# Performance work log

Measured on AMD Instinct MI355X. Metric: run time of the kernel, lower is better.

Reference implementation:

```python
import jax, jax.numpy as jnp
import numpy as np

N = 20000   # nodes
E = 320000  # edges per meta-path
F = 256     # input feature dim
H = 8       # attention heads
D = 64      # out dim per head
M = 2       # meta-paths
C = 5       # classes
HID = 128   # semantic attention hidden


def setup_inputs():
    key = jax.random.key(0)
    ks = jax.random.split(key, 12)
    s_in = 1.0 / np.sqrt(F)
    s_sem = 1.0 / np.sqrt(H * D)
    return {
        "h": jax.random.normal(ks[0], (N, F), jnp.float32),
        "src": jax.random.randint(ks[1], (M, E), 0, N, dtype=jnp.int32),
        "dst": jax.random.randint(ks[2], (M, E), 0, N, dtype=jnp.int32),
        "W": jax.random.normal(ks[3], (M, F, H * D), jnp.float32) * s_in,
        "attn_l": jax.random.normal(ks[4], (M, H, D), jnp.float32) * 0.1,
        "attn_r": jax.random.normal(ks[5], (M, H, D), jnp.float32) * 0.1,
        "bias_g": jnp.zeros((M, H * D), jnp.float32),
        "sem_W1": jax.random.normal(ks[6], (H * D, HID), jnp.float32) * s_sem,
        "sem_b1": jnp.zeros((HID,), jnp.float32),
        "sem_W2": jax.random.normal(ks[7], (HID, 1), jnp.float32) * (1.0 / np.sqrt(HID)),
        "pred_W": jax.random.normal(ks[8], (H * D, C), jnp.float32) * s_sem,
        "pred_b": jnp.zeros((C,), jnp.float32),
    }


def _gat_metapath(h, src, dst, W, al, ar, b):
    # DGL GATConv (allow_zero_in_degree=True), dropout disabled.
    feat = (h @ W).reshape(N, H, D)                     # [N,H,D]
    el = jnp.einsum("nhd,hd->nh", feat, al)             # [N,H]
    er = jnp.einsum("nhd,hd->nh", feat, ar)
    e = jax.nn.leaky_relu(el[src] + er[dst], 0.2)       # [E,H]
    # edge softmax over destination neighborhoods
    m = jax.ops.segment_max(e, dst, num_segments=N)
    m = jax.lax.stop_gradient(jnp.where(jnp.isfinite(m), m, 0.0))
    ex = jnp.exp(e - m[dst])
    den = jax.ops.segment_sum(ex, dst, num_segments=N)
    alpha = ex / jnp.maximum(den[dst], 1e-9)            # [E,H]
    # scatter-aggregate messages
    out = jax.ops.segment_sum(alpha[:, :, None] * feat[src], dst, num_segments=N)  # [N,H,D]
    out = jax.nn.elu(out + b.reshape(1, H, D))          # bias then activation (elu)
    return out.reshape(N, H * D)


def reference(h, src, dst, W, attn_l, attn_r, bias_g, sem_W1, sem_b1, sem_W2, pred_W, pred_b):
    # one GATConv per meta-path, flattened heads
    z = jnp.stack(
        [_gat_metapath(h, src[i], dst[i], W[i], attn_l[i], attn_r[i], bias_g[i]) for i in range(M)],
        axis=1,
    )  # [N, M, H*D]
    # semantic attention pooling over meta-paths
    w = jnp.tanh(z @ sem_W1 + sem_b1) @ sem_W2          # [N,M,1]
    beta = jax.nn.softmax(w.mean(0), axis=0)            # [M,1]
    hout = (beta[None] * z).sum(1)                      # [N,H*D]
    return hout @ pred_W + pred_b                        # [N,C]
```

## Files before the change

### kernel.cpp

```cpp
#include <hip/hip_runtime.h>
#include <hip/hip_bf16.h>

#define NN  20000
#define FF  256
#define HH  8
#define DD  64
#define HD  512
#define MM  2
#define EE  320000
#define CC  5
#define HID 128

#define GEMM_BLOCKS 1252
#define LP 40

typedef __attribute__((ext_vector_type(8))) short short8;
typedef __attribute__((ext_vector_type(4))) float f32x4;

__device__ __forceinline__ short f2bs(float v) {
  __hip_bfloat16 b = __float2bfloat16(v);
  return *reinterpret_cast<short*>(&b);
}
__device__ __forceinline__ int clampi(int v, int lo, int hi) {
  return v < lo ? lo : (v > hi ? hi : v);
}
__device__ __forceinline__ void bf8_unpack(uint4 u, float f[8]) {
  f[0] = __uint_as_float(u.x << 16); f[1] = __uint_as_float(u.x & 0xffff0000u);
  f[2] = __uint_as_float(u.y << 16); f[3] = __uint_as_float(u.y & 0xffff0000u);
  f[4] = __uint_as_float(u.z << 16); f[5] = __uint_as_float(u.z & 0xffff0000u);
  f[6] = __uint_as_float(u.w << 16); f[7] = __uint_as_float(u.w & 0xffff0000u);
}

__global__ __launch_bounds__(256) void convert_k(
    const float* __restrict__ W, const float* __restrict__ W1,
    const float* __restrict__ predW, const int* __restrict__ dst,
    __hip_bfloat16* __restrict__ Wt, __hip_bfloat16* __restrict__ W1t,
    __hip_bfloat16* __restrict__ predWt, int* __restrict__ counts,
    float* __restrict__ wsum)
{
  const int bid = blockIdx.x, tid = threadIdx.x;
  __shared__ short T[64 * 65];
  if (bid < 64) {
    int m = bid >> 5, t = bid & 31;
    int k0 = (t >> 3) * 64, c0 = (t & 7) * 64;
    const float* src = W + (size_t)m * FF * HD;
#pragma unroll
    for (int rr = 0; rr < 16; ++rr) {
      int idx = rr * 256 + tid;
      int r = idx >> 6, c = idx & 63;
      T[c * 65 + r] = f2bs(src[(size_t)(k0 + r) * HD + c0 + c]);
    }
    __syncthreads();
    __hip_bfloat16* dstp = Wt + (size_t)m * HD * FF;
#pragma unroll
    for (int rr = 0; rr < 16; ++rr) {
      int idx = rr * 256 + tid;
      int c = idx >> 6, k = idx & 63;
      dstp[(size_t)(c0 + c) * FF + k0 + k] = *reinterpret_cast<__hip_bfloat16*>(&T[c * 65 + k]);
    }
  } else if (bid < 80) {
    int t = bid - 64;
    int k0 = (t >> 1) * 64, c0 = (t & 1) * 64;
#pragma unroll
    for (int rr = 0; rr < 16; ++rr) {
      int idx = rr * 256 + tid;
      int r = idx >> 6, c = idx & 63;
      T[c * 65 + r] = f2bs(W1[(size_t)(k0 + r) * HID + c0 + c]);
    }
    __syncthreads();
#pragma unroll
    for (int rr = 0; rr < 16; ++rr) {
      int idx = rr * 256 + tid;
      int c = idx >> 6, k = idx & 63;
      W1t[(size_t)(c0 + c) * HD + k0 + k] = *reinterpret_cast<__hip_bfloat16*>(&T[c * 65 + k]);
    }
  } else if (bid == 80) {
    for (int i = tid; i < 16 * HD; i += 256) {
      int c = i >> 9, k = i & 511;
      predWt[i] = __float2bfloat16((c < CC) ? predW[(size_t)k * CC + c] : 0.f);
    }
    if (tid < 64) wsum[tid] = 0.f;
  } else {
    int e = (bid - 81) * 256 + tid;
    if (e < MM * EE) {
      int m = e / EE;
      int d = clampi(dst[e], 0, NN - 1);
      atomicAdd(&counts[m * NN + d], 1);
    }
  }
}

__global__ __launch_bounds__(256) void scan_k(const int* __restrict__ counts,
                                              int* __restrict__ offsets,
                                              int* __restrict__ cursor)
{
  const int m = blockIdx.x;
  const int tid = threadIdx.x;
  const int CH = (NN + 255) / 256;
  const int lo = tid * CH;
  const int hi = min(NN, lo + CH);
  __shared__ int sdata[256];
  int s = 0;
  for (int i = lo; i < hi; ++i) s += counts[m * NN + i];
  const int own = s;
  sdata[tid] = s;
  __syncthreads();
#pragma unroll
  for (int off = 1; off < 256; off <<= 1) {
    int v = (tid >= off) ? sdata[tid - off] : 0;
    __syncthreads();
    sdata[tid] += v;
    __syncthreads();
  }
  int run = sdata[tid] - own;
  for (int i = lo; i < hi; ++i) {
    offsets[m * (NN + 1) + i] = run;
    cursor[m * NN + i] = run;
    run += counts[m * NN + i];
  }
  if (tid == 255) offsets[m * (NN + 1) + NN] = sdata[255];
}

__global__ __launch_bounds__(256) void work_k(
    const float* __restrict__ h, const __hip_bfloat16* __restrict__ Wt,
    const float* __restrict__ al, const float* __restrict__ ar,
    const int* __restrict__ dst, const int* __restrict__ src,
    int* __restrict__ cursor, int* __restrict__ sidx,
    __hip_bfloat16* __restrict__ feat, float* __restrict__ el, float* __restrict__ er)
{
  if (blockIdx.x >= GEMM_BLOCKS) {
    int e = (blockIdx.x - GEMM_BLOCKS) * 256 + (int)threadIdx.x;
    if (e < MM * EE) {
      int m = e / EE;
      int d = clampi(dst[e], 0, NN - 1);
      int pos = atomicAdd(&cursor[m * NN + d], 1);
      sidx[(size_t)m * EE + pos] = clampi(src[e], 0, NN - 1);
    }
    return;
  }
  const int m    = blockIdx.x & 1;
  const int half = (blockIdx.x >> 1) & 1;
  const int row0 = (blockIdx.x >> 2) * 64;
  const int cb   = half * 256;
  const int tid  = threadIdx.x;
  const int wave = tid >> 6, lane = tid & 63;
  const int l15  = lane & 15, quad = lane >> 4;
  __shared__ __align__(16) short As[64 * LP];
  __shared__ __align__(16) short Bs[256 * LP];
  f32x4 acc[16];
#pragma unroll
  for (int i = 0; i < 16; ++i) acc[i] = (f32x4){0.f, 0.f, 0.f, 0.f};
  const __hip_bfloat16* Wtm = Wt + (size_t)m * HD * FF;

  for (int k0 = 0; k0 < FF; k0 += 32) {
    {
      int r = tid >> 2, kg = tid & 3;
      int row = row0 + r;
      short sv[8];
      if (row < NN) {
        const float* hp = h + (size_t)row * FF + k0 + kg * 8;
        float4 x = *(const float4*)hp, y = *(const float4*)(hp + 4);
        sv[0]=f2bs(x.x); sv[1]=f2bs(x.y); sv[2]=f2bs(x.z); sv[3]=f2bs(x.w);
        sv[4]=f2bs(y.x); sv[5]=f2bs(y.y); sv[6]=f2bs(y.z); sv[7]=f2bs(y.w);
      } else {
#pragma unroll
        for (int j = 0; j < 8; ++j) sv[j] = 0;
      }
      *(uint4*)(&As[r * LP + kg * 8]) = *(uint4*)sv;
    }
#pragma unroll
    for (int jj = 0; jj < 4; ++jj) {
      int idx = jj * 256 + tid;
      int c = idx >> 2, kg = idx & 3;
      *(uint4*)(&Bs[c * LP + kg * 8]) =
          *(const uint4*)(Wtm + (size_t)(cb + c) * FF + k0 + kg * 8);
    }
    __syncthreads();
    short8 a = *(const short8*)(&As[(16 * wave + l15) * LP + quad * 8]);
#pragma unroll
    for (int nt = 0; nt < 16; ++nt) {
      short8 b = *(const short8*)(&Bs[(nt * 16 + l15) * LP + quad * 8]);
      acc[nt] = __builtin_amdgcn_mfma_f32_16x16x32_bf16(a, b, acc[nt], 0, 0, 0);
    }
    __syncthreads();
  }
#pragma unroll
  for (int nt = 0; nt < 16; ++nt)
#pragma unroll
    for (int r = 0; r < 4; ++r) {
      int row = row0 + 16 * wave + quad * 4 + r;
      if (row < NN)
        feat[(size_t)m * NN * HD + (size_t)row * HD + cb + nt * 16 + l15] =
            __float2bfloat16(acc[nt][r]);
    }
#pragma unroll
  for (int lh = 0; lh < 4; ++lh) {
    const int hh2 = half * 4 + lh;
    float alv[4], arv[4];
#pragma unroll
    for (int t = 0; t < 4; ++t) {
      size_t ai = (size_t)m * HD + hh2 * 64 + t * 16 + l15;
      alv[t] = al[ai];
      arv[t] = ar[ai];
    }
#pragma unroll
    for (int r = 0; r < 4; ++r) {
      int row = row0 + 16 * wave + quad * 4 + r;
      float sl = 0.f, sr = 0.f;
#pragma unroll
      for (int t = 0; t < 4; ++t) {
        sl += acc[lh * 4 + t][r] * alv[t];
        sr += acc[lh * 4 + t][r] * arv[t];
      }
#pragma unroll
      for (int s = 1; s < 16; s <<= 1) {
        sl += __shfl_xor(sl, s);
        sr += __shfl_xor(sr, s);
      }
      if (l15 == 0 && row < NN) {
        el[((size_t)m * NN + row) * 8 + hh2] = sl;
        er[((size_t)m * NN + row) * 8 + hh2] = sr;
      }
    }
  }
}

__global__ __launch_bounds__(512) void aggregate_k(
    const int* __restrict__ sidx, const int* __restrict__ offsets,
    const float* __restrict__ el, const float* __restrict__ er,
    const __hip_bfloat16* __restrict__ feat, const float* __restrict__ bias_g,
    __hip_bfloat16* __restrict__ z)
{
  const int m = blockIdx.y;
  const int wave = threadIdx.x >> 6, lane = threadIdx.x & 63;
  const int n = blockIdx.x * 8 + wave;
  if (n >= NN) return;
  const int hh = lane >> 3;
  const int off = offsets[m * (NN + 1) + n];
  const int end = offsets[m * (NN + 1) + n + 1];
  const float er_h = er[((size_t)m * NN + n) * 8 + hh];
  const float* elm = el + (size_t)m * NN * 8;
  const int* sx = sidx + (size_t)m * EE;
  const __hip_bfloat16* fb = feat + (size_t)m * NN * HD + lane * 8;

  float acc[8];
#pragma unroll
  for (int j = 0; j < 8; ++j) acc[j] = 0.f;
  float den = 0.f;

  for (int base = off; base < end; base += 64) {
    const int cnt = min(64, end - base);
    int s_l = 0;
    if (lane < cnt) s_l = clampi(sx[base + lane], 0, NN - 1);
    int s_cur = __shfl(s_l, 0);
    uint4 u_cur = *(const uint4*)(fb + (size_t)s_cur * HD);
    float e_cur = elm[s_cur * 8 + hh];
    for (int i = 0; i < cnt; ++i) {
      int s_nxt = 0; uint4 u_nxt; float e_nxt = 0.f;
      if (i + 1 < cnt) {
        s_nxt = __shfl(s_l, i + 1);
        u_nxt = *(const uint4*)(fb + (size_t)s_nxt * HD);
        e_nxt = elm[s_nxt * 8 + hh];
      }
      float v = e_cur + er_h;
      v = v > 0.f ? v : 0.2f * v;
      float w = __expf(v);
      den += w;
      float f[8];
      bf8_unpack(u_cur, f);
#pragma unroll
      for (int j = 0; j < 8; ++j) acc[j] += w * f[j];
      s_cur = s_nxt; u_cur = u_nxt; e_cur = e_nxt;
    }
  }
  const float invden = 1.0f / fmaxf(den, 1e-9f);
  short sv[8];
#pragma unroll
  for (int j = 0; j < 8; ++j) {
    float o = acc[j] * invden + bias_g[(size_t)m * HD + lane * 8 + j];
    o = o > 0.f ? o : expm1f(o);
    sv[j] = f2bs(o);
  }
  *(uint4*)(z + ((size_t)m * NN + n) * HD + lane * 8) = *(uint4*)sv;
}

__global__ __launch_bounds__(256) void gemm_sem_k(
    const __hip_bfloat16* __restrict__ z, const __hip_bfloat16* __restrict__ W1t,
    const __hip_bfloat16* __restrict__ predWt,
    const float* __restrict__ b1, const float* __restrict__ W2,
    float* __restrict__ wsum, float* __restrict__ y)
{
  const int row0 = blockIdx.x * 64;
  const int tid  = threadIdx.x;
  const int wave = tid >> 6, lane = tid & 63;
  const int l15  = lane & 15, quad = lane >> 4;
  __shared__ __align__(16) short As[64 * LP];
  __shared__ __align__(16) short Bs[128 * LP];
  __shared__ float s_part[2];
  if (tid < 2) s_part[tid] = 0.f;
  f32x4 acc[8], accy;
#pragma unroll
  for (int i = 0; i < 8; ++i) acc[i] = (f32x4){0.f, 0.f, 0.f, 0.f};
  accy = (f32x4){0.f, 0.f, 0.f, 0.f};

  for (int k0 = 0; k0 < HD; k0 += 32) {
    {
      int r = tid >> 2, kg = tid & 3;
      *(uint4*)(&As[r * LP + kg * 8]) =
          *(const uint4*)(z + (size_t)(row0 + r) * HD + k0 + kg * 8);
    }
#pragma unroll
    for (int jj = 0; jj < 2; ++jj) {
      int idx = jj * 256 + tid;
      int c = idx >> 2, kg = idx & 3;
      *(uint4*)(&Bs[c * LP + kg * 8]) =
          *(const uint4*)(W1t + (size_t)c * HD + k0 + kg * 8);
    }
    __syncthreads();
    short8 a = *(const short8*)(&As[(16 * wave + l15) * LP + quad * 8]);
#pragma unroll
    for (int nt = 0; nt < 8; ++nt) {
      short8 b = *(const short8*)(&Bs[(nt * 16 + l15) * LP + quad * 8]);
      acc[nt] = __builtin_amdgcn_mfma_f32_16x16x32_bf16(a, b, acc[nt], 0, 0, 0);
    }
    short8 by = *(const short8*)(predWt + (size_t)l15 * HD + k0 + quad * 8);
    accy = __builtin_amdgcn_mfma_f32_16x16x32_bf16(a, by, accy, 0, 0, 0);
    __syncthreads();
  }
  float b1v[8], w2v[8];
#pragma unroll
  for (int nt = 0; nt < 8; ++nt) {
    int col = nt * 16 + l15;
    b1v[nt] = b1[col];
    w2v[nt] = W2[col];
  }
#pragma unroll
  for (int r = 0; r < 4; ++r) {
    float val = 0.f;
#pragma unroll
    for (int nt = 0; nt < 8; ++nt) val += tanhf(acc[nt][r] + b1v[nt]) * w2v[nt];
#pragma unroll
    for (int s = 1; s < 16; s <<= 1) val += __shfl_xor(val, s);
    if (l15 == 0) {
      int flat = row0 + 16 * wave + quad * 4 + r;
      atomicAdd(&s_part[flat / NN], val);
    }
  }
#pragma unroll
  for (int r = 0; r < 4; ++r) {
    int flat = row0 + 16 * wave + quad * 4 + r;
    if (l15 < CC) y[(size_t)flat * CC + l15] = accy[r];
  }
  __syncthreads();
  if (tid < 2 && s_part[tid] != 0.f) atomicAdd(&wsum[tid], s_part[tid]);
}

__global__ __launch_bounds__(256) void final_k(
    const float* __restrict__ y, const float* __restrict__ wsum,
    const float* __restrict__ predb, float* __restrict__ out)
{
  int i = blockIdx.x * 256 + threadIdx.x;
  if (i >= NN * CC) return;
  float s0 = wsum[0] * (1.0f / NN), s1 = wsum[1] * (1.0f / NN);
  float mx = fmaxf(s0, s1);
  float e0 = __expf(s0 - mx), e1 = __expf(s1 - mx);
  float inv = 1.0f / (e0 + e1);
  out[i] = (e0 * inv) * y[i] + (e1 * inv) * y[(size_t)NN * CC + i] + predb[i % CC];
}

extern "C" void kernel_launch(void* const* d_in, const int* in_sizes, int n_in,
                              void* d_out, int out_size, void* d_ws, size_t ws_size,
                              hipStream_t stream)
{
  const float* h      = (const float*)d_in[0];
  const int*   src    = (const int*)d_in[1];
  const int*   dst    = (const int*)d_in[2];
  const float* W      = (const float*)d_in[3];
  const float* al     = (const float*)d_in[4];
  const float* ar     = (const float*)d_in[5];
  const float* bias_g = (const float*)d_in[6];
  const float* semW1  = (const float*)d_in[7];
  const float* semb1  = (const float*)d_in[8];
  const float* semW2  = (const float*)d_in[9];
  const float* predW  = (const float*)d_in[10];
  const float* predb  = (const float*)d_in[11];

  char* p = (char*)d_ws;
  auto alloc = [&](size_t bytes) {
    char* r = p;
    p += (bytes + 255) & ~(size_t)255;
    return r;
  };
  int*   counts = (int*)alloc((size_t)MM * NN * 4);
  float* wsum   = (float*)alloc(256);
  int*   cursor = (int*)alloc((size_t)MM * NN * 4);
  float* el     = (float*)alloc((size_t)MM * NN * HH * 4);
  float* er     = (float*)alloc((size_t)MM * NN * HH * 4);
  int*   offs   = (int*)alloc((size_t)MM * (NN + 1) * 4);
  int*   sidx   = (int*)alloc((size_t)MM * EE * 4);
  float* y      = (float*)alloc((size_t)MM * NN * CC * 4);
  __hip_bfloat16* Wt     = (__hip_bfloat16*)alloc((size_t)MM * FF * HD * 2);
  __hip_bfloat16* W1t    = (__hip_bfloat16*)alloc((size_t)HD * HID * 2);
  __hip_bfloat16* predWt = (__hip_bfloat16*)alloc((size_t)16 * HD * 2);
  __hip_bfloat16* feat   = (__hip_bfloat16*)alloc((size_t)MM * NN * HD * 2);
  __hip_bfloat16* z      = (__hip_bfloat16*)alloc((size_t)MM * NN * HD * 2);

  hipMemsetAsync(counts, 0, (size_t)MM * NN * 4 + 256, stream);

  convert_k<<<2581, 256, 0, stream>>>(W, semW1, predW, dst, Wt, W1t, predWt, counts, wsum);
  scan_k<<<MM, 256, 0, stream>>>(counts, offs, cursor);
  work_k<<<GEMM_BLOCKS + (MM * EE + 255) / 256, 256, 0, stream>>>(
      h, Wt, al, ar, dst, src, cursor, sidx, feat, el, er);
  aggregate_k<<<dim3((NN + 7) / 8, MM), 512, 0, stream>>>(sidx, offs, el, er, feat, bias_g, z);
  gemm_sem_k<<<(MM * NN) / 64, 256, 0, stream>>>(z, W1t, predWt, semb1, semW2, wsum, y);
  final_k<<<(NN * CC + 255) / 256, 256, 0, stream>>>(y, wsum, predb, (float*)d_out);
}
```

Measured before the change: 347.4 us.

## Fuse edge aggregation with semantic-attention GEMM via shared-memory z tile

Merges the aggregation kernel and the semantic-attention/prediction GEMM into one kernel. Each 1024-thread block aggregates 16 nodes into a shared-memory bf16 tile, then 9 waves run MFMA against W1 and the prediction weights directly from that tile. This removes the global write and reread of z (about 41 MB) and one kernel launch. In exchange the blocks are larger, 7 of 16 waves sit idle during the GEMM phase, and B operands are read uncached from global per block.

```diff
diff --git a/kernel.cpp b/kernel.cpp
--- a/kernel.cpp
+++ b/kernel.cpp
@@ -13,6 +13,7 @@
 
 #define GEMM_BLOCKS 1252
 #define LP 40
+#define ZP 520
 
 typedef __attribute__((ext_vector_type(8))) short short8;
 typedef __attribute__((ext_vector_type(4))) float f32x4;
@@ -225,17 +226,22 @@
   }
 }
 
-__global__ __launch_bounds__(512) void aggregate_k(
+__global__ __launch_bounds__(1024) void aggsem_k(
     const int* __restrict__ sidx, const int* __restrict__ offsets,
     const float* __restrict__ el, const float* __restrict__ er,
     const __hip_bfloat16* __restrict__ feat, const float* __restrict__ bias_g,
-    __hip_bfloat16* __restrict__ z)
+    const __hip_bfloat16* __restrict__ W1t, const __hip_bfloat16* __restrict__ predWt,
+    const float* __restrict__ b1, const float* __restrict__ W2,
+    float* __restrict__ wsum, float* __restrict__ y)
 {
   const int m = blockIdx.y;
   const int wave = threadIdx.x >> 6, lane = threadIdx.x & 63;
-  const int n = blockIdx.x * 8 + wave;
-  if (n >= NN) return;
+  const int n = blockIdx.x * 16 + wave;
   const int hh = lane >> 3;
+  const int l15 = lane & 15, quad = lane >> 4;
+  __shared__ __align__(16) short zbuf[16 * ZP];
+  __shared__ float part[8][16];
+
   const int off = offsets[m * (NN + 1) + n];
   const int end = offsets[m * (NN + 1) + n + 1];
   const float er_h = er[((size_t)m * NN + n) * 8 + hh];
@@ -281,78 +287,46 @@
     o = o > 0.f ? o : expm1f(o);
     sv[j] = f2bs(o);
   }
-  *(uint4*)(z + ((size_t)m * NN + n) * HD + lane * 8) = *(uint4*)sv;
-}
-
-__global__ __launch_bounds__(256) void gemm_sem_k(
-    const __hip_bfloat16* __restrict__ z, const __hip_bfloat16* __restrict__ W1t,
-    const __hip_bfloat16* __restrict__ predWt,
-    const float* __restrict__ b1, const float* __restrict__ W2,
-    float* __restrict__ wsum, float* __restrict__ y)
-{
-  const int row0 = blockIdx.x * 64;
-  const int tid  = threadIdx.x;
-  const int wave = tid >> 6, lane = tid & 63;
-  const int l15  = lane & 15, quad = lane >> 4;
-  __shared__ __align__(16) short As[64 * LP];
-  __shared__ __align__(16) short Bs[128 * LP];
-  __shared__ float s_part[2];
-  if (tid < 2) s_part[tid] = 0.f;
-  f32x4 acc[8], accy;
-#pragma unroll
-  for (int i = 0; i < 8; ++i) acc[i] = (f32x4){0.f, 0.f, 0.f, 0.f};
-  accy = (f32x4){0.f, 0.f, 0.f, 0.f};
-
-  for (int k0 = 0; k0 < HD; k0 += 32) {
-    {
-      int r = tid >> 2, kg = tid & 3;
-      *(uint4*)(&As[r * LP + kg * 8]) =
-          *(const uint4*)(z + (size_t)(row0 + r) * HD + k0 + kg * 8);
-    }
-#pragma unroll
-    for (int jj = 0; jj < 2; ++jj) {
-      int idx = jj * 256 + tid;
-      int c = idx >> 2, kg = idx & 3;
-      *(uint4*)(&Bs[c * LP + kg * 8]) =
-          *(const uint4*)(W1t + (size_t)c * HD + k0 + kg * 8);
-    }
-    __syncthreads();
-    short8 a = *(const short8*)(&As[(16 * wave + l15) * LP + quad * 8]);
-#pragma unroll
-    for (int nt = 0; nt < 8; ++nt) {
-      short8 b = *(const short8*)(&Bs[(nt * 16 + l15) * LP + quad * 8]);
-      acc[nt] = __builtin_amdgcn_mfma_f32_16x16x32_bf16(a, b, acc[nt], 0, 0, 0);
-    }
-    short8 by = *(const short8*)(predWt + (size_t)l15 * HD + k0 + quad * 8);
-    accy = __builtin_amdgcn_mfma_f32_16x16x32_bf16(a, by, accy, 0, 0, 0);
-    __syncthreads();
-  }
-  float b1v[8], w2v[8];
-#pragma unroll
-  for (int nt = 0; nt < 8; ++nt) {
-    int col = nt * 16 + l15;
-    b1v[nt] = b1[col];
-    w2v[nt] = W2[col];
-  }
-#pragma unroll
-  for (int r = 0; r < 4; ++r) {
-    float val = 0.f;
-#pragma unroll
-    for (int nt = 0; nt < 8; ++nt) val += tanhf(acc[nt][r] + b1v[nt]) * w2v[nt];
-#pragma unroll
-    for (int s = 1; s < 16; s <<= 1) val += __shfl_xor(val, s);
-    if (l15 == 0) {
-      int flat = row0 + 16 * wave + quad * 4 + r;
-      atomicAdd(&s_part[flat / NN], val);
-    }
-  }
-#pragma unroll
-  for (int r = 0; r < 4; ++r) {
-    int flat = row0 + 16 * wave + quad * 4 + r;
-    if (l15 < CC) y[(size_t)flat * CC + l15] = accy[r];
-  }
+  *(uint4*)(&zbuf[wave * ZP + lane * 8]) = *(uint4*)sv;
   __syncthreads();
-  if (tid < 2 && s_part[tid] != 0.f) atomicAdd(&wsum[tid], s_part[tid]);
+
+  if (wave < 9) {
+    const __hip_bfloat16* Bsrc = (wave < 8)
+        ? (W1t + (size_t)(wave * 16 + l15) * HD)
+        : (predWt + (size_t)l15 * HD);
+    f32x4 c = (f32x4){0.f, 0.f, 0.f, 0.f};
+    for (int k0 = 0; k0 < HD; k0 += 32) {
+      short8 a = *(const short8*)(&zbuf[l15 * ZP + k0 + quad * 8]);
+      short8 b = *(const short8*)(Bsrc + k0 + quad * 8);
+      c = __builtin_amdgcn_mfma_f32_16x16x32_bf16(a, b, c, 0, 0, 0);
+    }
+    if (wave < 8) {
+      float b1v = b1[wave * 16 + l15];
+      float w2v = W2[wave * 16 + l15];
+#pragma unroll
+      for (int r = 0; r < 4; ++r) {
+        float v = tanhf(c[r] + b1v) * w2v;
+#pragma unroll
+        for (int s = 1; s < 16; s <<= 1) v += __shfl_xor(v, s);
+        if (l15 == 0) part[wave][quad * 4 + r] = v;
+      }
+    } else {
+#pragma unroll
+      for (int r = 0; r < 4; ++r) {
+        int node = blockIdx.x * 16 + quad * 4 + r;
+        if (l15 < CC) y[((size_t)m * NN + node) * CC + l15] = c[r];
+      }
+    }
+  }
+  __syncthreads();
+  if (wave == 0 && lane < 16) {
+    float s = 0.f;
+#pragma unroll
+    for (int w = 0; w < 8; ++w) s += part[w][lane];
+#pragma unroll
+    for (int sft = 1; sft < 16; sft <<= 1) s += __shfl_xor(s, sft);
+    if (lane == 0) atomicAdd(&wsum[m], s);
+  }
 }
 
 __global__ __launch_bounds__(256) void final_k(
@@ -403,7 +377,6 @@
   __hip_bfloat16* W1t    = (__hip_bfloat16*)alloc((size_t)HD * HID * 2);
   __hip_bfloat16* predWt = (__hip_bfloat16*)alloc((size_t)16 * HD * 2);
   __hip_bfloat16* feat   = (__hip_bfloat16*)alloc((size_t)MM * NN * HD * 2);
-  __hip_bfloat16* z      = (__hip_bfloat16*)alloc((size_t)MM * NN * HD * 2);
 
   hipMemsetAsync(counts, 0, (size_t)MM * NN * 4 + 256, stream);
 
@@ -411,7 +384,7 @@
   scan_k<<<MM, 256, 0, stream>>>(counts, offs, cursor);
   work_k<<<GEMM_BLOCKS + (MM * EE + 255) / 256, 256, 0, stream>>>(
       h, Wt, al, ar, dst, src, cursor, sidx, feat, el, er);
-  aggregate_k<<<dim3((NN + 7) / 8, MM), 512, 0, stream>>>(sidx, offs, el, er, feat, bias_g, z);
-  gemm_sem_k<<<(MM * NN) / 64, 256, 0, stream>>>(z, W1t, predWt, semb1, semW2, wsum, y);
+  aggsem_k<<<dim3(NN / 16, MM), 1024, 0, stream>>>(
+      sidx, offs, el, er, feat, bias_g, W1t, predWt, semb1, semW2, wsum, y);
   final_k<<<(NN * CC + 255) / 256, 256, 0, stream>>>(y, wsum, predb, (float*)d_out);
 }
```

Result: slower. 365.9 us (+5.3%).
